# Optimization experiments

Hardware: AMD Instinct MI355X
Metric: run time of the kernel (lower is better)

## Reference

```python
import math
import jax, jax.numpy as jnp
import numpy as np

B, T, D, M, S = 2, 4096, 1024, 256, 8
BEAM = 4
TAU = 1.0


def setup_inputs() -> dict:
    key = jax.random.key(0)
    ks = jax.random.split(key, 24)
    std = 0.02
    inp = {
        "mu": jax.random.normal(ks[0], (B, T, D), jnp.float32),
        "lam": jax.random.uniform(ks[1], (B, T, D), jnp.float32),
        "pi": jax.random.uniform(ks[2], (B, T, 7), jnp.float32),
        "pi_write": jax.random.uniform(ks[3], (B, T, 1), jnp.float32),
        "Wq": jax.random.normal(ks[4], (M, D), jnp.float32) * std,
        "bq": jnp.zeros((M,), jnp.float32),
        "Wk": jax.random.normal(ks[5], (M, D), jnp.float32) * std,
        "bk": jnp.zeros((M,), jnp.float32),
        "Wv": jax.random.normal(ks[6], (M, D), jnp.float32) * std,
        "bv": jnp.zeros((M,), jnp.float32),
        "Wo": jax.random.normal(ks[7], (D, M), jnp.float32) * std,
        "bo": jnp.zeros((D,), jnp.float32),
        "Ws1": jax.random.normal(ks[8], (256, 2 * D + 7), jnp.float32) * std,
        "bs1": jnp.zeros((256,), jnp.float32),
        "Ws2": jax.random.normal(ks[9], (1, 256), jnp.float32) * std,
        "bs2": jnp.zeros((1,), jnp.float32),
        "Wsr": jax.random.normal(ks[10], (M, M), jnp.float32) * std,
        "bsr": jnp.zeros((M,), jnp.float32),
        "scratch_init": jax.random.normal(ks[11], (1, S, M), jnp.float32) * 0.02,
        "gate": jnp.float32(-5.0),
    }
    return inp


def _build_tree(k, v, w):
    """Causal binary tree of weighted span summaries. Level 0 = leaves."""
    levels = [(k, v, w)]
    while k.shape[1] > 1:
        n = k.shape[1]
        if n % 2 == 1:
            pad = ((0, 0), (0, 1), (0, 0))
            k = jnp.pad(k, pad); v = jnp.pad(v, pad); w = jnp.pad(w, pad)
        k1, k2 = k[:, 0::2], k[:, 1::2]
        v1, v2 = v[:, 0::2], v[:, 1::2]
        w1, w2 = w[:, 0::2], w[:, 1::2]
        tw = w1 + w2 + 1e-8
        k = (w1 * k1 + w2 * k2) / tw
        v = (w1 * v1 + w2 * v2) / tw
        w = tw
        levels.append((k, v, w))
    return levels


def _retrieve_at_level(q, keys, values, beam):
    Bq, Tq, Mq = q.shape
    n = keys.shape[1]
    scores = jnp.einsum('btm,bnm->btn', q, keys) / math.sqrt(Mq)
    if n <= Tq:  # causal: query i may only see slot j <= i
        mask = jnp.arange(n)[None, :] > jnp.arange(Tq)[:, None]
        scores = jnp.where(mask[None], -jnp.inf, scores)
    kk = min(beam, n)
    if n > kk:
        vals, idx = jax.lax.top_k(scores, kk)           # (B,T,k)
        p = jax.nn.softmax(vals, axis=-1)               # == softmax of scattered sparse scores
        v_sel = jnp.take_along_axis(values[:, None], idx[..., None], axis=2)  # (B,T,k,M)
        return jnp.einsum('btk,btkm->btm', p, v_sel)
    attn = jax.nn.softmax(scores, axis=-1)
    return jnp.einsum('btn,bnm->btm', attn, values)


def reference(mu, lam, pi, pi_write, Wq, bq, Wk, bk, Wv, bv, Wo, bo,
              Ws1, bs1, Ws2, bs2, Wsr, bsr, scratch_init, gate):
    # ---- write: build causal tree from detached keys/values ----
    mu_d = jax.lax.stop_gradient(mu)
    w0 = jax.lax.stop_gradient(pi_write)                # (B,T,1)
    k = mu_d @ Wk.T + bk
    v = mu_d @ Wv.T + bv
    tree = _build_tree(k, v, w0)

    # ---- read ----
    q = mu @ Wq.T + bq                                  # (B,T,M)
    log_var = -jnp.log(jnp.clip(lam, 1e-6))
    si = jnp.concatenate([mu, log_var, pi], axis=-1)    # (B,T,2D+7)
    h = si @ Ws1.T + bs1
    h = h * jax.nn.sigmoid(h)                           # SiLU
    s = jax.nn.sigmoid((h @ Ws2.T + bs2)[..., 0])       # (B,T)

    scratch = jnp.broadcast_to(scratch_init, (mu.shape[0], S, M))
    sq = q @ Wsr.T + bsr
    sattn = jax.nn.softmax(jnp.einsum('btm,bsm->bts', sq, scratch) / math.sqrt(M), axis=-1)
    scratch_ctx = jnp.einsum('bts,bsm->btm', sattn, scratch)

    level_ctx = [_retrieve_at_level(q, lk, lv, BEAM) for (lk, lv, _) in tree]
    level_stack = jnp.stack(level_ctx, axis=2)          # (B,T,L,M)
    L = level_stack.shape[2]
    level_idx = jnp.arange(L, dtype=mu.dtype)
    s_scaled = s[..., None] * (L - 1)                   # (B,T,1)
    kappa = jnp.exp(-0.5 * ((level_idx - s_scaled) / TAU) ** 2)
    kappa = kappa / jnp.clip(kappa.sum(axis=-1, keepdims=True), 1e-8)
    tree_ctx = jnp.einsum('btl,btlm->btm', kappa, level_stack)

    blend = s[..., None]
    combined = (1.0 - blend) * tree_ctx + blend * scratch_ctx
    out = combined @ Wo.T + bo
    return jax.nn.sigmoid(gate) * out                   # (B,T,D)
```

## Files before the change

### kernel.cpp

```cpp
#include <hip/hip_runtime.h>
#include <math.h>

#define TT 4096
#define BB 2
#define MMDIM 256
#define RTOT 8192
#define NSLICE 39

typedef __attribute__((ext_vector_type(8))) short short8_t;
typedef __attribute__((ext_vector_type(4))) float f32x4;

template<int WITH_GATE>
__global__ __launch_bounds__(256) void gemm_f32(
    const float* __restrict__ A, const float* __restrict__ W,
    const float* __restrict__ bias, const float* __restrict__ gate,
    float* __restrict__ C, int K, int N)
{
    __shared__ float As[16][68];
    __shared__ float Ws[16][68];
    const int tid = threadIdx.x;
    const int tx = tid & 15, ty = tid >> 4;
    const int r0 = blockIdx.x * 64, c0 = blockIdx.y * 64;
    const int lr = tid >> 2;
    const int lk = (tid & 3) << 2;

    float acc[4][4] = {};

    for (int k0 = 0; k0 < K; k0 += 16) {
        float4 av = *(const float4*)&A[(size_t)(r0 + lr) * K + k0 + lk];
        float4 wv = *(const float4*)&W[(size_t)(c0 + lr) * K + k0 + lk];
        As[lk + 0][lr] = av.x; As[lk + 1][lr] = av.y;
        As[lk + 2][lr] = av.z; As[lk + 3][lr] = av.w;
        Ws[lk + 0][lr] = wv.x; Ws[lk + 1][lr] = wv.y;
        Ws[lk + 2][lr] = wv.z; Ws[lk + 3][lr] = wv.w;
        __syncthreads();
        #pragma unroll
        for (int kk = 0; kk < 16; ++kk) {
            float4 a = *(const float4*)&As[kk][ty * 4];
            float4 b = *(const float4*)&Ws[kk][tx * 4];
            acc[0][0] += a.x * b.x; acc[0][1] += a.x * b.y; acc[0][2] += a.x * b.z; acc[0][3] += a.x * b.w;
            acc[1][0] += a.y * b.x; acc[1][1] += a.y * b.y; acc[1][2] += a.y * b.z; acc[1][3] += a.y * b.w;
            acc[2][0] += a.z * b.x; acc[2][1] += a.z * b.y; acc[2][2] += a.z * b.z; acc[2][3] += a.z * b.w;
            acc[3][0] += a.w * b.x; acc[3][1] += a.w * b.y; acc[3][2] += a.w * b.z; acc[3][3] += a.w * b.w;
        }
        __syncthreads();
    }

    float g = 1.f;
    if (WITH_GATE) g = 1.f / (1.f + expf(-gate[0]));
    #pragma unroll
    for (int i = 0; i < 4; ++i) {
        int row = r0 + ty * 4 + i;
        float4 o;
        o.x = (acc[i][0] + bias[c0 + tx * 4 + 0]) * g;
        o.y = (acc[i][1] + bias[c0 + tx * 4 + 1]) * g;
        o.z = (acc[i][2] + bias[c0 + tx * 4 + 2]) * g;
        o.w = (acc[i][3] + bias[c0 + tx * 4 + 3]) * g;
        *(float4*)&C[(size_t)row * N + c0 + tx * 4] = o;
    }
}

__device__ __forceinline__ unsigned short f2bf(float x)
{
    unsigned u = __float_as_uint(x);
    u += 0x7fffu + ((u >> 16) & 1u);
    return (unsigned short)(u >> 16);
}

__global__ __launch_bounds__(256) void convert_split(
    const float* __restrict__ src, unsigned short* __restrict__ hi,
    unsigned short* __restrict__ lo, int n4)
{
    int i = blockIdx.x * 256 + threadIdx.x;
    if (i >= n4) return;
    float4 x = ((const float4*)src)[i];
    ushort4 h, l;
    h.x = f2bf(x.x); l.x = f2bf(x.x - __uint_as_float((unsigned)h.x << 16));
    h.y = f2bf(x.y); l.y = f2bf(x.y - __uint_as_float((unsigned)h.y << 16));
    h.z = f2bf(x.z); l.z = f2bf(x.z - __uint_as_float((unsigned)h.z << 16));
    h.w = f2bf(x.w); l.w = f2bf(x.w - __uint_as_float((unsigned)h.w << 16));
    ((ushort4*)hi)[i] = h;
    ((ushort4*)lo)[i] = l;
}

__global__ __launch_bounds__(256) void pad_ws1_split(
    const float* __restrict__ src, unsigned short* __restrict__ hi,
    unsigned short* __restrict__ lo)
{
    const int r = blockIdx.x;
    for (int c = threadIdx.x; c < 2112; c += 256) {
        float v = (c < 2055) ? src[(size_t)r * 2055 + c] : 0.f;
        unsigned short h = f2bf(v);
        hi[(size_t)r * 2112 + c] = h;
        lo[(size_t)r * 2112 + c] = f2bf(v - __uint_as_float((unsigned)h << 16));
    }
}

template<int ASRC, int WITH_GATE>
__global__ __launch_bounds__(256) void gemm_mfma(
    const float* __restrict__ A, const float* __restrict__ lam,
    const float* __restrict__ pi,
    const unsigned short* __restrict__ Wh, const unsigned short* __restrict__ Wl,
    const float* __restrict__ bias, const float* __restrict__ gate,
    float* __restrict__ C, int K, int N)
{
    __shared__ unsigned short Ah[64][72], Al[64][72];
    __shared__ unsigned short Bh[128][72], Bl[128][72];
    const int tid = threadIdx.x;
    const int lane = tid & 63;
    const int wv = tid >> 6;
    const int r0 = blockIdx.x * 64;
    const int c0 = blockIdx.y * 128;

    f32x4 acc0[8] = {}, acc1[8] = {}, acc2[8] = {};

    const int arow = wv * 16 + (lane & 15);
    const int koff = (lane >> 4) * 8;

    for (int kc = 0; kc < K; kc += 64) {
        #pragma unroll
        for (int i = 0; i < 2; ++i) {
            int g = tid + i * 256;
            int row = g >> 3, gq = g & 7;
            float x[8];
            if (ASRC == 0) {
                float4 v0 = *(const float4*)&A[(size_t)(r0 + row) * K + kc + gq * 8];
                float4 v1 = *(const float4*)&A[(size_t)(r0 + row) * K + kc + gq * 8 + 4];
// ... 29 lines not shown
            *(short8_t*)&Bl[row][gq * 8] = *(const short8_t*)&Wl[(size_t)(c0 + row) * K + kc + gq * 8];
        }
        __syncthreads();
        #pragma unroll
        for (int kt = 0; kt < 2; ++kt) {
            short8_t afh = *(const short8_t*)&Ah[arow][kt * 32 + koff];
            short8_t afl = *(const short8_t*)&Al[arow][kt * 32 + koff];
            #pragma unroll
            for (int ct = 0; ct < 8; ++ct) {
                short8_t bh = *(const short8_t*)&Bh[ct * 16 + (lane & 15)][kt * 32 + koff];
                short8_t bl = *(const short8_t*)&Bl[ct * 16 + (lane & 15)][kt * 32 + koff];
                acc0[ct] = __builtin_amdgcn_mfma_f32_16x16x32_bf16(afh, bh, acc0[ct], 0, 0, 0);
                acc1[ct] = __builtin_amdgcn_mfma_f32_16x16x32_bf16(afl, bh, acc1[ct], 0, 0, 0);
                acc2[ct] = __builtin_amdgcn_mfma_f32_16x16x32_bf16(afh, bl, acc2[ct], 0, 0, 0);
            }
        }
        __syncthreads();
    }

    float g = 1.f;
    if (WITH_GATE) g = 1.f / (1.f + expf(-gate[0]));
    #pragma unroll
    for (int ct = 0; ct < 8; ++ct) {
        int col = c0 + ct * 16 + (lane & 15);
        float b = bias[col];
        #pragma unroll
        for (int r = 0; r < 4; ++r) {
            int row = r0 + wv * 16 + (lane >> 4) * 4 + r;
            C[(size_t)row * N + col] = (acc0[ct][r] + acc1[ct][r] + acc2[ct][r] + b) * g;
        }
    }
}

__global__ __launch_bounds__(256) void s_kernel(
    const float* __restrict__ h, const float* __restrict__ Ws2,
    const float* __restrict__ bs2, float* __restrict__ sb,
    float* __restrict__ kap)
{
    const int tid = threadIdx.x;
    const int wave = tid >> 6, lane = tid & 63;
    const int t = blockIdx.x * 4 + wave;

    float4 hv = *(const float4*)&h[(size_t)t * MMDIM + lane * 4];
    float4 wv = *(const float4*)&Ws2[lane * 4];
    float p = 0.f;
    p += (hv.x / (1.f + expf(-hv.x))) * wv.x;
    p += (hv.y / (1.f + expf(-hv.y))) * wv.y;
    p += (hv.z / (1.f + expf(-hv.z))) * wv.z;
    p += (hv.w / (1.f + expf(-hv.w))) * wv.w;
    #pragma unroll
    for (int o = 32; o; o >>= 1) p += __shfl_xor(p, o);

    float z = p + bs2[0];
    float s = 1.f / (1.f + expf(-z));
    float c = s * 12.f;
    float Z = 0.f;
    #pragma unroll
    for (int l = 0; l < 13; ++l) {
        float d = (float)l - c;
        Z += expf(-0.5f * d * d);
    }
    Z = fmaxf(Z, 1e-8f);
    if (lane < 13) {
        float d = (float)lane - c;
        kap[(size_t)t * 16 + lane] = (1.f - s) * expf(-0.5f * d * d) / Z;
    }
    if (lane == 0) sb[t] = s;
}

__global__ __launch_bounds__(256) void scratch_kernel(
    const float* __restrict__ sq, const float* __restrict__ scr,
    const float* __restrict__ sb, float* __restrict__ ctx)
{
    const int tid = threadIdx.x;
    const int wave = tid >> 6, lane = tid & 63;
    const int t = blockIdx.x * 4 + wave;

    float4 qv = *(const float4*)&sq[(size_t)t * MMDIM + lane * 4];
    float4 fr[8];
    float sc[8];
    #pragma unroll
    for (int s = 0; s < 8; ++s) {
        fr[s] = *(const float4*)&scr[s * MMDIM + lane * 4];
        sc[s] = qv.x * fr[s].x + qv.y * fr[s].y + qv.z * fr[s].z + qv.w * fr[s].w;
    }
    #pragma unroll
    for (int s = 0; s < 8; ++s) {
        #pragma unroll
        for (int o = 32; o; o >>= 1) sc[s] += __shfl_xor(sc[s], o);
        sc[s] *= 0.0625f;
    }
    float mx = sc[0];
    #pragma unroll
    for (int s = 1; s < 8; ++s) mx = fmaxf(mx, sc[s]);
    float sum = 0.f;
    #pragma unroll
    for (int s = 0; s < 8; ++s) { sc[s] = expf(sc[s] - mx); sum += sc[s]; }
    float inv = 1.f / sum;
    float blend = sb[t];
    float4 o = {0, 0, 0, 0};
    #pragma unroll
    for (int s = 0; s < 8; ++s) {
        float pp = sc[s] * inv;
        o.x += pp * fr[s].x; o.y += pp * fr[s].y;
        o.z += pp * fr[s].z; o.w += pp * fr[s].w;
    }
    o.x *= blend; o.y *= blend; o.z *= blend; o.w *= blend;
    *(float4*)&ctx[(size_t)t * MMDIM + lane * 4] = o;
}

__global__ __launch_bounds__(256) void wtree_kernel(
    const float* __restrict__ pw, float* __restrict__ wtree)
{
    __shared__ float wa[4096];
    __shared__ float wb2[2048];
    const int b = blockIdx.x;
    const int tid = threadIdx.x;
    for (int t = tid; t < 4096; t += 256) wa[t] = pw[b * 4096 + t];
    __syncthreads();
    int n = 4096, lvl = 1;
    float* cur = wa; float* nxt = wb2;
    while (n > 1) {
        int nout = n >> 1;
        int off = TT - (8192 >> lvl);
        for (int j = tid; j < nout; j += 256) {
            float t = cur[2 * j] + cur[2 * j + 1] + 1e-8f;
            nxt[j] = t;
            wtree[b * 4095 + off + j] = t;
        }
        __syncthreads();
        float* tmp = cur; cur = nxt; nxt = tmp;
        n = nout; ++lvl;
    }
}

__global__ __launch_bounds__(256) void tree_level(
    const float* __restrict__ kin, const float* __restrict__ vin,
    const float* __restrict__ win, float* __restrict__ kout,
    float* __restrict__ vout, int in_bs, int win_bs, int out_bs)
{
    const int j = blockIdx.x;
    const int b = blockIdx.y;
    const int tid = threadIdx.x;
    const float* wp = win + (size_t)b * win_bs;
    float w1 = wp[2 * j], w2 = wp[2 * j + 1];
    float tw = w1 + w2 + 1e-8f;
    size_t i1 = ((size_t)b * in_bs + 2 * j) * MMDIM + tid;
    size_t io = ((size_t)b * out_bs + j) * MMDIM + tid;
    kout[io] = (w1 * kin[i1] + w2 * kin[i1 + MMDIM]) / tw;
    vout[io] = (w1 * vin[i1] + w2 * vin[i1 + MMDIM]) / tw;
}

__global__ __launch_bounds__(256) void tree_deep(
    float* __restrict__ kt_, float* __restrict__ vt_,
    const float* __restrict__ wtree)
{
    __shared__ float kb[128][68];
    __shared__ float vb[128][68];
    const int tid = threadIdx.x;
    const int mc = blockIdx.x;
    const int b = blockIdx.y;
    const int wb = b * 4095;

    for (int idx = tid; idx < 64 * 64; idx += 256) {
        int j = idx >> 6, m = idx & 63;
        size_t gi = (size_t)(wb + 3968 + j) * MMDIM + mc * 64 + m;
        kb[j][m] = kt_[gi];
        vb[j][m] = vt_[gi];
    }
    __syncthreads();

    int pb = 0;
    for (int l = 7; l <= 12; ++l) {
        int nout = 4096 >> l;
        int cb = 128 - (128 >> (l - 6));
        int offm1 = TT - (8192 >> (l - 1));
        int offl  = TT - (8192 >> l);
        for (int idx = tid; idx < nout * 64; idx += 256) {
            int j = idx >> 6, m = idx & 63;
            float w1 = wtree[wb + offm1 + 2 * j];
            float w2 = wtree[wb + offm1 + 2 * j + 1];
            float tw = wtree[wb + offl + j];
            float kvv = (w1 * kb[pb + 2 * j][m] + w2 * kb[pb + 2 * j + 1][m]) / tw;
            float vvv = (w1 * vb[pb + 2 * j][m] + w2 * vb[pb + 2 * j + 1][m]) / tw;
            kb[cb + j][m] = kvv;
            vb[cb + j][m] = vvv;
            size_t go = (size_t)(wb + offl + j) * MMDIM + mc * 64 + m;
            kt_[go] = kvv;
            vt_[go] = vvv;
        }
        __syncthreads();
        pb = cb;
    }
}

__device__ __forceinline__ bool beats(float v, int id, float v2, int id2)
{
    return (v > v2) || (v == v2 && id < id2);
}

__device__ __forceinline__ void ins4(float v, int id, float tv[4], int ti[4])
{
    if (!beats(v, id, tv[3], ti[3])) return;
    tv[3] = v; ti[3] = id;
    #pragma unroll
    for (int s = 3; s > 0; --s) {
        if (beats(tv[s], ti[s], tv[s - 1], ti[s - 1])) {
            float fv = tv[s]; tv[s] = tv[s - 1]; tv[s - 1] = fv;
            int iv = ti[s]; ti[s] = ti[s - 1]; ti[s - 1] = iv;
        }
    }
}

__device__ __forceinline__ void ins5(float v, int id, float tv[5], int ti[5])
{
    if (!beats(v, id, tv[4], ti[4])) return;
    tv[4] = v; ti[4] = id;
    #pragma unroll
    for (int s = 4; s > 0; --s) {
        if (beats(tv[s], ti[s], tv[s - 1], ti[s - 1])) {
            float fv = tv[s]; tv[s] = tv[s - 1]; tv[s - 1] = fv;
            int iv = ti[s]; ti[s] = ti[s - 1]; ti[s - 1] = iv;
        }
    }
}

__device__ __forceinline__ void slice_map(int sid, int& level, int& c0)
{
    if (sid < 16)      { level = 0; c0 = sid << 8; }
    else if (sid < 24) { level = 1; c0 = (sid - 16) << 8; }
    else if (sid < 28) { level = 2; c0 = (sid - 24) << 8; }
    else if (sid < 30) { level = 3; c0 = (sid - 28) << 8; }
    else               { level = sid - 26; c0 = 0; }
}

__global__ __launch_bounds__(256) void topk_mfma(
    const unsigned short* __restrict__ qkh, const unsigned short* __restrict__ qkl,
    const unsigned short* __restrict__ kth, const unsigned short* __restrict__ ktl,
    float2* __restrict__ topw)
{
    __shared__ unsigned short kbh[32][264];
    __shared__ unsigned short kbl[32][264];

    const int tid = threadIdx.x;
    const int lane = tid & 63;
    const int wv = tid >> 6;
    const int r0 = blockIdx.x * 64;
    const int sid = blockIdx.y;
    const int b = r0 >> 12;
    const int t0 = r0 & 4095;

    int level, c0b;
    slice_map(sid, level, c0b);
    const int n = TT >> level;
    const int nv = min(min(n, t0 + 64), c0b + 256);

    if (c0b >= nv) {
        if (tid < 64) {
            float2 e = make_float2(-INFINITY, __int_as_float(0x7fffffff));
            #pragma unroll
            for (int s = 0; s < 5; ++s)
                topw[(size_t)(sid * 5 + s) * RTOT + r0 + tid] = e;
        }
        return;
    }

    const unsigned short* Kh;
    const unsigned short* Kl;
    if (level == 0) {
        Kh = qkh + (size_t)RTOT * MMDIM + (size_t)b * TT * MMDIM;
        Kl = qkl + (size_t)RTOT * MMDIM + (size_t)b * TT * MMDIM;
    } else {
        size_t off = (size_t)b * 4095 + (TT - (8192 >> level));
        Kh = kth + off * MMDIM;
        Kl = ktl + off * MMDIM;
    }

    const int arow = r0 + wv * 16 + (lane & 15);
    const int koff = (lane >> 4) * 8;
    short8_t ah[8], al[8];
    #pragma unroll
    for (int kt = 0; kt < 8; ++kt) {
        ah[kt] = *(const short8_t*)(qkh + (size_t)arow * MMDIM + kt * 32 + koff);
        al[kt] = *(const short8_t*)(qkl + (size_t)arow * MMDIM + kt * 32 + koff);
    }

    float tv[4][4];
    int ti[4][4];
    #pragma unroll
    for (int r = 0; r < 4; ++r)
        #pragma unroll
        for (int s = 0; s < 4; ++s) { tv[r][s] = -INFINITY; ti[r][s] = 0x7fffffff; }

    const int scol = tid >> 3;
    const int kseg = (tid & 7) * 32;

    for (int c0 = c0b; c0 < nv; c0 += 32) {
        {
            int cc = min(c0 + scol, n - 1);
            const unsigned short* gh = Kh + (size_t)cc * MMDIM + kseg;
            const unsigned short* gl = Kl + (size_t)cc * MMDIM + kseg;
            #pragma unroll
            for (int i = 0; i < 4; ++i) {
                *(short8_t*)&kbh[scol][kseg + i * 8] = *(const short8_t*)(gh + i * 8);
                *(short8_t*)&kbl[scol][kseg + i * 8] = *(const short8_t*)(gl + i * 8);
            }
        }
        __syncthreads();

        #pragma unroll
        for (int ct = 0; ct < 2; ++ct) {
            f32x4 a0 = {0.f, 0.f, 0.f, 0.f};
            f32x4 a1 = {0.f, 0.f, 0.f, 0.f};
            f32x4 a2 = {0.f, 0.f, 0.f, 0.f};
            const int bc = ct * 16 + (lane & 15);
            #pragma unroll
            for (int kt = 0; kt < 8; ++kt) {
                short8_t bh = *(const short8_t*)&kbh[bc][kt * 32 + koff];
                short8_t bl = *(const short8_t*)&kbl[bc][kt * 32 + koff];
                a0 = __builtin_amdgcn_mfma_f32_16x16x32_bf16(ah[kt], bh, a0, 0, 0, 0);
                a1 = __builtin_amdgcn_mfma_f32_16x16x32_bf16(al[kt], bh, a1, 0, 0, 0);
                a2 = __builtin_amdgcn_mfma_f32_16x16x32_bf16(ah[kt], bl, a2, 0, 0, 0);
            }
            const int col = c0 + bc;
            #pragma unroll
            for (int r = 0; r < 4; ++r) {
                int trow = t0 + wv * 16 + (lane >> 4) * 4 + r;
                float cand = (col <= trow && col < n)
                    ? (a0[r] + a1[r] + a2[r]) * 0.0625f : -INFINITY;
                if (__any(cand > tv[r][3])) ins4(cand, col, tv[r], ti[r]);
            }
        }
        __syncthreads();
    }

    #pragma unroll
    for (int r = 0; r < 4; ++r) {
        float v5[5]; int i5[5];
        #pragma unroll
        for (int s = 0; s < 4; ++s) { v5[s] = tv[r][s]; i5[s] = ti[r][s]; }
        v5[4] = -INFINITY; i5[4] = 0x7fffffff;
        #pragma unroll
        for (int pass = 0; pass < 4; ++pass) {
            int off = 1 << pass;
            float ov[5]; int oi[5];
            #pragma unroll
            for (int s = 0; s < 5; ++s) {
                ov[s] = __shfl_xor(v5[s], off);
                oi[s] = __shfl_xor(i5[s], off);
            }
            #pragma unroll
            for (int s = 0; s < 5; ++s) ins5(ov[s], oi[s], v5, i5);
        }
        if ((lane & 15) == 0) {
            int row = r0 + wv * 16 + (lane >> 4) * 4 + r;
            #pragma unroll
            for (int s = 0; s < 5; ++s)
                topw[(size_t)(sid * 5 + s) * RTOT + row] =
                    make_float2(v5[s], __int_as_float(i5[s]));
        }
    }
}

__global__ __launch_bounds__(256) void merge_gather(
    const float2* __restrict__ topw, const float* __restrict__ q,
    const float* __restrict__ kl0, const float* __restrict__ ktf,
    const float* __restrict__ vl0, const float* __restrict__ vtree,
    const float* __restrict__ kap, float* __restrict__ ctx)
{
    const int tid = threadIdx.x;
    const int lane = tid & 63;
    const int wv = __builtin_amdgcn_readfirstlane(tid >> 6);
    const int row = blockIdx.x * 4 + wv;
    const int b = row >> 12;

    float cr[4] = {0, 0, 0, 0};
    const float4 q4 = *(const float4*)&q[(size_t)row * MMDIM + lane * 4];

    for (int l = 0; l <= 12; ++l) {
        int s0, cnt;
        if (l == 0)      { s0 = 0;  cnt = 16; }
        else if (l == 1) { s0 = 16; cnt = 8; }
        else if (l == 2) { s0 = 24; cnt = 4; }
        else if (l == 3) { s0 = 28; cnt = 2; }
        else             { s0 = 26 + l; cnt = 1; }

        float tv[5]; int ti[5];
        #pragma unroll
        for (int s = 0; s < 5; ++s) { tv[s] = -INFINITY; ti[s] = 0x7fffffff; }
        for (int sl = 0; sl < cnt; ++sl) {
            #pragma unroll
            for (int s = 0; s < 5; ++s) {
// ... 81 lines not shown
    const float* bs2 = (const float*)d_in[15];
    const float* Wsr = (const float*)d_in[16];
    const float* bsr = (const float*)d_in[17];
    const float* scr = (const float*)d_in[18];
    const float* gate = (const float*)d_in[19];
    float* out = (float*)d_out;

    float* w = (float*)d_ws;
    const size_t RM = (size_t)RTOT * MMDIM;
    float* q_   = w;  w += RM;
    float* k_   = w;  w += RM;
    float* v_   = w;  w += RM;
    float* h_   = w;  w += RM;
    float* sq_  = w;  w += RM;
    float* ctx_ = w;  w += RM;
    float* sb_  = w;  w += RTOT;
    float* kap_ = w;  w += (size_t)RTOT * 16;
    float* kt_  = w;  w += (size_t)BB * 4095 * MMDIM;
    float* vt_  = w;  w += (size_t)BB * 4095 * MMDIM;
    float* wtree_ = w; w += (size_t)BB * 4095;
    unsigned short* qkh_ = (unsigned short*)w;  w += RM;
    unsigned short* qkl_ = (unsigned short*)w;  w += RM;
    unsigned short* kth_ = (unsigned short*)w;  w += (size_t)BB * 4095 * MMDIM / 2;
    unsigned short* ktl_ = (unsigned short*)w;  w += (size_t)BB * 4095 * MMDIM / 2;
    float2* topw = (float2*)w;  w += (size_t)NSLICE * 5 * RTOT * 2;
    unsigned short* w1h_ = (unsigned short*)w;  w += (size_t)256 * 2112 / 2;
    unsigned short* w1l_ = (unsigned short*)w;  w += (size_t)256 * 2112 / 2;
    unsigned short* wvh_ = (unsigned short*)w;  w += (size_t)256 * 1024 / 2;
    unsigned short* wvl_ = (unsigned short*)w;  w += (size_t)256 * 1024 / 2;
    unsigned short* wsrh_ = (unsigned short*)w; w += (size_t)256 * 256 / 2;
    unsigned short* wsrl_ = (unsigned short*)w; w += (size_t)256 * 256 / 2;
    unsigned short* woh_ = (unsigned short*)w;  w += (size_t)1024 * 256 / 2;
    unsigned short* wol_ = (unsigned short*)w;  w += (size_t)1024 * 256 / 2;

    pad_ws1_split<<<256, 256, 0, stream>>>(Ws1, w1h_, w1l_);
    convert_split<<<256, 256, 0, stream>>>(Wv, wvh_, wvl_, 65536);
    convert_split<<<64, 256, 0, stream>>>(Wsr, wsrh_, wsrl_, 16384);
    convert_split<<<256, 256, 0, stream>>>(Wo, woh_, wol_, 65536);

    gemm_f32<0><<<dim3(128, 4), 256, 0, stream>>>(mu, Wq, bq, nullptr, q_, 1024, 256);
    gemm_f32<0><<<dim3(128, 4), 256, 0, stream>>>(mu, Wk, bk, nullptr, k_, 1024, 256);
    gemm_mfma<0, 0><<<dim3(128, 2), 256, 0, stream>>>(mu, nullptr, nullptr, wvh_, wvl_,
                                                      bv, nullptr, v_, 1024, 256);
    gemm_mfma<1, 0><<<dim3(128, 2), 256, 0, stream>>>(mu, lam, pi, w1h_, w1l_,
                                                      bs1, nullptr, h_, 2112, 256);
    s_kernel<<<2048, 256, 0, stream>>>(h_, Ws2, bs2, sb_, kap_);
    gemm_mfma<0, 0><<<dim3(128, 2), 256, 0, stream>>>(q_, nullptr, nullptr, wsrh_, wsrl_,
                                                      bsr, nullptr, sq_, 256, 256);
    scratch_kernel<<<2048, 256, 0, stream>>>(sq_, scr, sb_, ctx_);

    wtree_kernel<<<BB, 256, 0, stream>>>(pw, wtree_);
    {
        const float* kin = k_; const float* vin = v_; const float* win = pw;
        int in_bs = TT, win_bs = TT;
        for (int l = 1; l <= 6; ++l) {
            int nout = TT >> l;
            int off = TT - (8192 >> l);
            float* ko = kt_ + (size_t)off * MMDIM;
            float* vo = vt_ + (size_t)off * MMDIM;
            tree_level<<<dim3(nout, BB), 256, 0, stream>>>(kin, vin, win, ko, vo,
                                                           in_bs, win_bs, 4095);
            kin = ko; vin = vo; win = wtree_ + off;
            in_bs = 4095; win_bs = 4095;
        }
    }
    tree_deep<<<dim3(4, BB), 256, 0, stream>>>(kt_, vt_, wtree_);

    convert_split<<<(int)((2 * RM / 4 + 255) / 256), 256, 0, stream>>>(
        q_, qkh_, qkl_, (int)(2 * RM / 4));
    convert_split<<<(int)(((size_t)BB * 4095 * MMDIM / 4 + 255) / 256), 256, 0, stream>>>(
        kt_, kth_, ktl_, (int)((size_t)BB * 4095 * MMDIM / 4));

    topk_mfma<<<dim3(128, NSLICE), 256, 0, stream>>>(qkh_, qkl_, kth_, ktl_, topw);
    merge_gather<<<2048, 256, 0, stream>>>(topw, q_, k_, kt_, v_, vt_, kap_, ctx_);
    gemm_mfma<0, 1><<<dim3(128, 8), 256, 0, stream>>>(ctx_, nullptr, nullptr, woh_, wol_,
                                                      bo, gate, out, 256, 1024);
}
```

Before: 873.2 us.

## Pack top-k keys into 64-bit ints, fuse tree levels, double topk block rows

The top-k insertion now stores each score and column together in one order-preserving 64-bit key, so comparisons are single integer compares and the shuffle merge moves one value per entry instead of two. The topk kernel processes 128 query rows per 512-thread block, so each staged K tile is reused across twice as many rows. The per-level tree_level launches for levels 2-6 are replaced by one tree_mid kernel that reduces a 64-leaf group in shared memory, removing five launches and the global round-trips between them. The unused gate template is dropped from gemm_f32. Risks are the larger block lowering occupancy, 64-bit shuffle cost, and the reproduction of tie-breaking through the packed key encoding.

```diff
diff --git a/kernel.cpp b/kernel.cpp
--- a/kernel.cpp
+++ b/kernel.cpp
@@ -10,11 +10,9 @@
 typedef __attribute__((ext_vector_type(8))) short short8_t;
 typedef __attribute__((ext_vector_type(4))) float f32x4;
 
-template<int WITH_GATE>
 __global__ __launch_bounds__(256) void gemm_f32(
     const float* __restrict__ A, const float* __restrict__ W,
-    const float* __restrict__ bias, const float* __restrict__ gate,
-    float* __restrict__ C, int K, int N)
+    const float* __restrict__ bias, float* __restrict__ C, int K, int N)
 {
     __shared__ float As[16][68];
     __shared__ float Ws[16][68];
@@ -46,16 +44,14 @@
         __syncthreads();
     }
 
-    float g = 1.f;
-    if (WITH_GATE) g = 1.f / (1.f + expf(-gate[0]));
     #pragma unroll
     for (int i = 0; i < 4; ++i) {
         int row = r0 + ty * 4 + i;
         float4 o;
-        o.x = (acc[i][0] + bias[c0 + tx * 4 + 0]) * g;
-        o.y = (acc[i][1] + bias[c0 + tx * 4 + 1]) * g;
-        o.z = (acc[i][2] + bias[c0 + tx * 4 + 2]) * g;
-        o.w = (acc[i][3] + bias[c0 + tx * 4 + 3]) * g;
+        o.x = acc[i][0] + bias[c0 + tx * 4 + 0];
+        o.y = acc[i][1] + bias[c0 + tx * 4 + 1];
+        o.z = acc[i][2] + bias[c0 + tx * 4 + 2];
+        o.w = acc[i][3] + bias[c0 + tx * 4 + 3];
         *(float4*)&C[(size_t)row * N + c0 + tx * 4] = o;
     }
 }
@@ -307,6 +303,51 @@
     vout[io] = (w1 * vin[i1] + w2 * vin[i1 + MMDIM]) / tw;
 }
 
+__global__ __launch_bounds__(256) void tree_mid(
+    float* __restrict__ kt_, float* __restrict__ vt_,
+    const float* __restrict__ wtree)
+{
+    __shared__ float kb[128][68];
+    __shared__ float vb[128][68];
+    const int tid = threadIdx.x;
+    const int g  = blockIdx.x >> 2;
+    const int mc = blockIdx.x & 3;
+    const int b  = blockIdx.y;
+    const int wb = b * 4095;
+
+    for (int idx = tid; idx < 64 * 64; idx += 256) {
+        int j = idx >> 6, m = idx & 63;
+        size_t gi = (size_t)(wb + g * 64 + j) * MMDIM + mc * 64 + m;
+        kb[j][m] = kt_[gi];
+        vb[j][m] = vt_[gi];
+    }
+    __syncthreads();
+
+    int pb = 0;
+    for (int l = 2; l <= 6; ++l) {
+        int nloc = 64 >> (l - 1);
+        int cb = 128 - (128 >> (l - 1));
+        int offm1 = TT - (8192 >> (l - 1));
+        int offl  = TT - (8192 >> l);
+        int gbase = g * nloc;
+        for (int idx = tid; idx < nloc * 64; idx += 256) {
+            int j = idx >> 6, m = idx & 63;
+            float w1 = wtree[wb + offm1 + (gbase + j) * 2];
+            float w2 = wtree[wb + offm1 + (gbase + j) * 2 + 1];
+            float tw = wtree[wb + offl + gbase + j];
+            float kvv = (w1 * kb[pb + 2 * j][m] + w2 * kb[pb + 2 * j + 1][m]) / tw;
+            float vvv = (w1 * vb[pb + 2 * j][m] + w2 * vb[pb + 2 * j + 1][m]) / tw;
+            kb[cb + j][m] = kvv;
+            vb[cb + j][m] = vvv;
+            size_t go = (size_t)(wb + offl + gbase + j) * MMDIM + mc * 64 + m;
+            kt_[go] = kvv;
+            vt_[go] = vvv;
+        }
+        __syncthreads();
+        pb = cb;
+    }
+}
+
 __global__ __launch_bounds__(256) void tree_deep(
     float* __restrict__ kt_, float* __restrict__ vt_,
     const float* __restrict__ wtree)
@@ -350,22 +391,50 @@
     }
 }
 
+__device__ __forceinline__ unsigned long long pack_key(float v, int col)
+{
+    unsigned u = __float_as_uint(v);
+    u ^= ((unsigned)((int)u >> 31)) | 0x80000000u;
+    return ((unsigned long long)u << 32) | (unsigned)(~col);
+}
+
+__device__ __forceinline__ void unpack_key(unsigned long long k, float& v, int& col)
+{
+    unsigned u = (unsigned)(k >> 32);
+    u ^= (u & 0x80000000u) ? 0x80000000u : 0xFFFFFFFFu;
+    v = __uint_as_float(u);
+    col = (int)(~(unsigned)k);
+}
+
+__device__ __forceinline__ unsigned long long shfl_xor_u64(unsigned long long v, int off)
+{
+    int lo = __shfl_xor((int)(unsigned)v, off);
+    int hi = __shfl_xor((int)(v >> 32), off);
+    return ((unsigned long long)(unsigned)hi << 32) | (unsigned)lo;
+}
+
+__device__ __forceinline__ void ins4u(unsigned long long k, unsigned long long t[4])
+{
+    if (k <= t[3]) return;
+    t[3] = k;
+    if (t[3] > t[2]) { unsigned long long x = t[2]; t[2] = t[3]; t[3] = x; }
+    if (t[2] > t[1]) { unsigned long long x = t[1]; t[1] = t[2]; t[2] = x; }
+    if (t[1] > t[0]) { unsigned long long x = t[0]; t[0] = t[1]; t[1] = x; }
+}
+
+__device__ __forceinline__ void ins5u(unsigned long long k, unsigned long long t[5])
+{
+    if (k <= t[4]) return;
+    t[4] = k;
+    if (t[4] > t[3]) { unsigned long long x = t[3]; t[3] = t[4]; t[4] = x; }
+    if (t[3] > t[2]) { unsigned long long x = t[2]; t[2] = t[3]; t[3] = x; }
+    if (t[2] > t[1]) { unsigned long long x = t[1]; t[1] = t[2]; t[2] = x; }
+    if (t[1] > t[0]) { unsigned long long x = t[0]; t[0] = t[1]; t[1] = x; }
+}
+
 __device__ __forceinline__ bool beats(float v, int id, float v2, int id2)
 {
     return (v > v2) || (v == v2 && id < id2);
-}
-
-__device__ __forceinline__ void ins4(float v, int id, float tv[4], int ti[4])
-{
-    if (!beats(v, id, tv[3], ti[3])) return;
-    tv[3] = v; ti[3] = id;
-    #pragma unroll
-    for (int s = 3; s > 0; --s) {
-        if (beats(tv[s], ti[s], tv[s - 1], ti[s - 1])) {
-            float fv = tv[s]; tv[s] = tv[s - 1]; tv[s - 1] = fv;
-            int iv = ti[s]; ti[s] = ti[s - 1]; ti[s - 1] = iv;
-        }
-    }
 }
 
 __device__ __forceinline__ void ins5(float v, int id, float tv[5], int ti[5])
@@ -390,7 +459,7 @@
     else               { level = sid - 26; c0 = 0; }
 }
 
-__global__ __launch_bounds__(256) void topk_mfma(
+__global__ __launch_bounds__(512) void topk_mfma(
     const unsigned short* __restrict__ qkh, const unsigned short* __restrict__ qkl,
     const unsigned short* __restrict__ kth, const unsigned short* __restrict__ ktl,
     float2* __restrict__ topw)
@@ -401,7 +470,7 @@
     const int tid = threadIdx.x;
     const int lane = tid & 63;
     const int wv = tid >> 6;
-    const int r0 = blockIdx.x * 64;
+    const int r0 = blockIdx.x * 128;
     const int sid = blockIdx.y;
     const int b = r0 >> 12;
     const int t0 = r0 & 4095;
@@ -409,10 +478,10 @@
     int level, c0b;
     slice_map(sid, level, c0b);
     const int n = TT >> level;
-    const int nv = min(min(n, t0 + 64), c0b + 256);
+    const int nv = min(min(n, t0 + 128), c0b + 256);
 
     if (c0b >= nv) {
-        if (tid < 64) {
+        if (tid < 128) {
             float2 e = make_float2(-INFINITY, __int_as_float(0x7fffffff));
             #pragma unroll
             for (int s = 0; s < 5; ++s)
@@ -441,26 +510,21 @@
         al[kt] = *(const short8_t*)(qkl + (size_t)arow * MMDIM + kt * 32 + koff);
     }
 
-    float tv[4][4];
-    int ti[4][4];
-    #pragma unroll
-    for (int r = 0; r < 4; ++r)
-        #pragma unroll
-        for (int s = 0; s < 4; ++s) { tv[r][s] = -INFINITY; ti[r][s] = 0x7fffffff; }
-
-    const int scol = tid >> 3;
-    const int kseg = (tid & 7) * 32;
+    unsigned long long tk[4][4] = {};
+    const int trow0 = t0 + wv * 16 + (lane >> 4) * 4;
+
+    const int scol = tid >> 4;
+    const int kseg = (tid & 15) * 16;
 
     for (int c0 = c0b; c0 < nv; c0 += 32) {
         {
             int cc = min(c0 + scol, n - 1);
             const unsigned short* gh = Kh + (size_t)cc * MMDIM + kseg;
             const unsigned short* gl = Kl + (size_t)cc * MMDIM + kseg;
-            #pragma unroll
-            for (int i = 0; i < 4; ++i) {
-                *(short8_t*)&kbh[scol][kseg + i * 8] = *(const short8_t*)(gh + i * 8);
-                *(short8_t*)&kbl[scol][kseg + i * 8] = *(const short8_t*)(gl + i * 8);
-            }
+            *(short8_t*)&kbh[scol][kseg]     = *(const short8_t*)gh;
+            *(short8_t*)&kbh[scol][kseg + 8] = *(const short8_t*)(gh + 8);
+            *(short8_t*)&kbl[scol][kseg]     = *(const short8_t*)gl;
+            *(short8_t*)&kbl[scol][kseg + 8] = *(const short8_t*)(gl + 8);
         }
         __syncthreads();
 
@@ -481,10 +545,10 @@
             const int col = c0 + bc;
             #pragma unroll
             for (int r = 0; r < 4; ++r) {
-                int trow = t0 + wv * 16 + (lane >> 4) * 4 + r;
-                float cand = (col <= trow && col < n)
-                    ? (a0[r] + a1[r] + a2[r]) * 0.0625f : -INFINITY;
-                if (__any(cand > tv[r][3])) ins4(cand, col, tv[r], ti[r]);
+                float sc = (a0[r] + a1[r] + a2[r]) * 0.0625f;
+                unsigned long long key =
+                    (col <= trow0 + r && col < n) ? pack_key(sc, col) : 0ull;
+                if (__any(key > tk[r][3])) ins4u(key, tk[r]);
             }
         }
         __syncthreads();
@@ -492,28 +556,33 @@
 
     #pragma unroll
     for (int r = 0; r < 4; ++r) {
-        float v5[5]; int i5[5];
-        #pragma unroll
-        for (int s = 0; s < 4; ++s) { v5[s] = tv[r][s]; i5[s] = ti[r][s]; }
-        v5[4] = -INFINITY; i5[4] = 0x7fffffff;
+        unsigned long long k5[5];
+        #pragma unroll
+        for (int s = 0; s < 4; ++s) k5[s] = tk[r][s];
+        k5[4] = 0ull;
         #pragma unroll
         for (int pass = 0; pass < 4; ++pass) {
             int off = 1 << pass;
-            float ov[5]; int oi[5];
-            #pragma unroll
-            for (int s = 0; s < 5; ++s) {
-                ov[s] = __shfl_xor(v5[s], off);
-                oi[s] = __shfl_xor(i5[s], off);
-            }
-            #pragma unroll
-            for (int s = 0; s < 5; ++s) ins5(ov[s], oi[s], v5, i5);
+            unsigned long long o[5];
+            #pragma unroll
+            for (int s = 0; s < 5; ++s) o[s] = shfl_xor_u64(k5[s], off);
+            #pragma unroll
+            for (int s = 0; s < 5; ++s) ins5u(o[s], k5);
         }
         if ((lane & 15) == 0) {
             int row = r0 + wv * 16 + (lane >> 4) * 4 + r;
             #pragma unroll
-            for (int s = 0; s < 5; ++s)
-                topw[(size_t)(sid * 5 + s) * RTOT + row] =
-                    make_float2(v5[s], __int_as_float(i5[s]));
+            for (int s = 0; s < 5; ++s) {
+                float2 e;
+                if (k5[s] == 0ull) {
+                    e = make_float2(-INFINITY, __int_as_float(0x7fffffff));
+                } else {
+                    float v; int c;
+                    unpack_key(k5[s], v, c);
+                    e = make_float2(v, __int_as_float(c));
+                }
+                topw[(size_t)(sid * 5 + s) * RTOT + row] = e;
+            }
         }
     }
 }
@@ -667,8 +736,8 @@
     convert_split<<<64, 256, 0, stream>>>(Wsr, wsrh_, wsrl_, 16384);
     convert_split<<<256, 256, 0, stream>>>(Wo, woh_, wol_, 65536);
 
-    gemm_f32<0><<<dim3(128, 4), 256, 0, stream>>>(mu, Wq, bq, nullptr, q_, 1024, 256);
-    gemm_f32<0><<<dim3(128, 4), 256, 0, stream>>>(mu, Wk, bk, nullptr, k_, 1024, 256);
+    gemm_f32<<<dim3(128, 4), 256, 0, stream>>>(mu, Wq, bq, q_, 1024, 256);
+    gemm_f32<<<dim3(128, 4), 256, 0, stream>>>(mu, Wk, bk, k_, 1024, 256);
     gemm_mfma<0, 0><<<dim3(128, 2), 256, 0, stream>>>(mu, nullptr, nullptr, wvh_, wvl_,
                                                       bv, nullptr, v_, 1024, 256);
     gemm_mfma<1, 0><<<dim3(128, 2), 256, 0, stream>>>(mu, lam, pi, w1h_, w1l_,
@@ -679,20 +748,9 @@
     scratch_kernel<<<2048, 256, 0, stream>>>(sq_, scr, sb_, ctx_);
 
     wtree_kernel<<<BB, 256, 0, stream>>>(pw, wtree_);
-    {
-        const float* kin = k_; const float* vin = v_; const float* win = pw;
-        int in_bs = TT, win_bs = TT;
-        for (int l = 1; l <= 6; ++l) {
-            int nout = TT >> l;
-            int off = TT - (8192 >> l);
-            float* ko = kt_ + (size_t)off * MMDIM;
-            float* vo = vt_ + (size_t)off * MMDIM;
-            tree_level<<<dim3(nout, BB), 256, 0, stream>>>(kin, vin, win, ko, vo,
-                                                           in_bs, win_bs, 4095);
-            kin = ko; vin = vo; win = wtree_ + off;
-            in_bs = 4095; win_bs = 4095;
-        }
-    }
+    tree_level<<<dim3(2048, BB), 256, 0, stream>>>(k_, v_, pw, kt_, vt_,
+                                                   TT, TT, 4095);
+    tree_mid<<<dim3(128, BB), 256, 0, stream>>>(kt_, vt_, wtree_);
     tree_deep<<<dim3(4, BB), 256, 0, stream>>>(kt_, vt_, wtree_);
 
     convert_split<<<(int)((2 * RM / 4 + 255) / 256), 256, 0, stream>>>(
@@ -700,7 +758,7 @@
     convert_split<<<(int)(((size_t)BB * 4095 * MMDIM / 4 + 255) / 256), 256, 0, stream>>>(
         kt_, kth_, ktl_, (int)((size_t)BB * 4095 * MMDIM / 4));
 
-    topk_mfma<<<dim3(128, NSLICE), 256, 0, stream>>>(qkh_, qkl_, kth_, ktl_, topw);
+    topk_mfma<<<dim3(64, NSLICE), 512, 0, stream>>>(qkh_, qkl_, kth_, ktl_, topw);
     merge_gather<<<2048, 256, 0, stream>>>(topw, q_, k_, kt_, v_, vt_, kap_, ctx_);
     gemm_mfma<0, 1><<<dim3(128, 8), 256, 0, stream>>>(ctx_, nullptr, nullptr, woh_, wol_,
                                                       bo, gate, out, 256, 1024);
```

After: 899.9 us. 1.03x slower.

## Fuse weight splits, Q/K GEMMs, s/scratch kernels, and tree levels into fewer launches

Applied to the files above, without the earlier changes.

Merges the four weight-splitting launches into one kernel and the separate Q and K FP32 GEMMs into one double-buffered GEMM that also emits the bf16 hi/lo split of q and k. The s and scratch kernels become a single kernel, which removes the sb round trip. The six per-level tree launches become one shared-memory tree_all kernel that writes the bf16 split inline, as tree_deep now does too, so the separate convert passes are gone. The aim is to cut launch overhead and redundant global traffic, at the cost of more complex kernels and a tree kernel that relies on large shared-memory buffers.

```diff
diff --git a/kernel.cpp b/kernel.cpp
--- a/kernel.cpp
+++ b/kernel.cpp
@@ -10,56 +10,6 @@
 typedef __attribute__((ext_vector_type(8))) short short8_t;
 typedef __attribute__((ext_vector_type(4))) float f32x4;
 
-template<int WITH_GATE>
-__global__ __launch_bounds__(256) void gemm_f32(
-    const float* __restrict__ A, const float* __restrict__ W,
-    const float* __restrict__ bias, const float* __restrict__ gate,
-    float* __restrict__ C, int K, int N)
-{
-    __shared__ float As[16][68];
-    __shared__ float Ws[16][68];
-    const int tid = threadIdx.x;
-    const int tx = tid & 15, ty = tid >> 4;
-    const int r0 = blockIdx.x * 64, c0 = blockIdx.y * 64;
-    const int lr = tid >> 2;
-    const int lk = (tid & 3) << 2;
-
-    float acc[4][4] = {};
-
-    for (int k0 = 0; k0 < K; k0 += 16) {
-        float4 av = *(const float4*)&A[(size_t)(r0 + lr) * K + k0 + lk];
-        float4 wv = *(const float4*)&W[(size_t)(c0 + lr) * K + k0 + lk];
-        As[lk + 0][lr] = av.x; As[lk + 1][lr] = av.y;
-        As[lk + 2][lr] = av.z; As[lk + 3][lr] = av.w;
-        Ws[lk + 0][lr] = wv.x; Ws[lk + 1][lr] = wv.y;
-        Ws[lk + 2][lr] = wv.z; Ws[lk + 3][lr] = wv.w;
-        __syncthreads();
-        #pragma unroll
-        for (int kk = 0; kk < 16; ++kk) {
-            float4 a = *(const float4*)&As[kk][ty * 4];
-            float4 b = *(const float4*)&Ws[kk][tx * 4];
-            acc[0][0] += a.x * b.x; acc[0][1] += a.x * b.y; acc[0][2] += a.x * b.z; acc[0][3] += a.x * b.w;
-            acc[1][0] += a.y * b.x; acc[1][1] += a.y * b.y; acc[1][2] += a.y * b.z; acc[1][3] += a.y * b.w;
-            acc[2][0] += a.z * b.x; acc[2][1] += a.z * b.y; acc[2][2] += a.z * b.z; acc[2][3] += a.z * b.w;
-            acc[3][0] += a.w * b.x; acc[3][1] += a.w * b.y; acc[3][2] += a.w * b.z; acc[3][3] += a.w * b.w;
-        }
-        __syncthreads();
-    }
-
-    float g = 1.f;
-    if (WITH_GATE) g = 1.f / (1.f + expf(-gate[0]));
-    #pragma unroll
-    for (int i = 0; i < 4; ++i) {
-        int row = r0 + ty * 4 + i;
-        float4 o;
-        o.x = (acc[i][0] + bias[c0 + tx * 4 + 0]) * g;
-        o.y = (acc[i][1] + bias[c0 + tx * 4 + 1]) * g;
-        o.z = (acc[i][2] + bias[c0 + tx * 4 + 2]) * g;
-        o.w = (acc[i][3] + bias[c0 + tx * 4 + 3]) * g;
-        *(float4*)&C[(size_t)row * N + c0 + tx * 4] = o;
-    }
-}
-
 __device__ __forceinline__ unsigned short f2bf(float x)
 {
     unsigned u = __float_as_uint(x);
@@ -67,12 +17,102 @@
     return (unsigned short)(u >> 16);
 }
 
-__global__ __launch_bounds__(256) void convert_split(
-    const float* __restrict__ src, unsigned short* __restrict__ hi,
-    unsigned short* __restrict__ lo, int n4)
-{
-    int i = blockIdx.x * 256 + threadIdx.x;
-    if (i >= n4) return;
+__global__ __launch_bounds__(256) void gemm_qk(
+    const float* __restrict__ mu, const float* __restrict__ Wq,
+    const float* __restrict__ bq, const float* __restrict__ Wk,
+    const float* __restrict__ bk, float* __restrict__ q_, float* __restrict__ k_,
+    unsigned short* __restrict__ qkh, unsigned short* __restrict__ qkl)
+{
+    __shared__ float As[2][8][68];
+    __shared__ float Ws[2][8][132];
+    const int tid = threadIdx.x;
+    const int tx = tid & 15;
+    const int ty = tid >> 4;
+    const int r0 = blockIdx.x * 64;
+    const int c0 = blockIdx.y * 128;
+    const bool isq = (c0 < 256);
+
+    const float* W = isq ? (Wq + (size_t)c0 * 1024)
+                         : (Wk + (size_t)(c0 - 256) * 1024);
+    const float* bias = isq ? (bq + c0) : (bk + (c0 - 256));
+
+    const bool isA = (tid < 128);
+    const int sArow = tid >> 1, sAk = (tid & 1) * 4;
+    const int sWrow = tid >> 1, sWk = (tid & 1) * 4;
+
+    float acc[4][8] = {};
+    float4 rA, rW;
+
+    if (isA) rA = *(const float4*)&mu[(size_t)(r0 + sArow) * 1024 + sAk];
+    rW = *(const float4*)&W[(size_t)sWrow * 1024 + sWk];
+    if (isA) {
+        As[0][sAk + 0][sArow] = rA.x; As[0][sAk + 1][sArow] = rA.y;
+        As[0][sAk + 2][sArow] = rA.z; As[0][sAk + 3][sArow] = rA.w;
+    }
+    Ws[0][sWk + 0][sWrow] = rW.x; Ws[0][sWk + 1][sWrow] = rW.y;
+    Ws[0][sWk + 2][sWrow] = rW.z; Ws[0][sWk + 3][sWrow] = rW.w;
+    __syncthreads();
+
+    int buf = 0;
+    for (int k0 = 0; k0 < 1024; k0 += 8) {
+        const bool has = (k0 + 8 < 1024);
+        if (has) {
+            if (isA) rA = *(const float4*)&mu[(size_t)(r0 + sArow) * 1024 + k0 + 8 + sAk];
+            rW = *(const float4*)&W[(size_t)sWrow * 1024 + k0 + 8 + sWk];
+        }
+        #pragma unroll
+        for (int kk = 0; kk < 8; ++kk) {
+            float4 a  = *(const float4*)&As[buf][kk][ty * 4];
+            float4 b0 = *(const float4*)&Ws[buf][kk][tx * 8];
+            float4 b1 = *(const float4*)&Ws[buf][kk][tx * 8 + 4];
+            float av[4] = {a.x, a.y, a.z, a.w};
+            float bv[8] = {b0.x, b0.y, b0.z, b0.w, b1.x, b1.y, b1.z, b1.w};
+            #pragma unroll
+            for (int i = 0; i < 4; ++i)
+                #pragma unroll
+                for (int j = 0; j < 8; ++j)
+                    acc[i][j] += av[i] * bv[j];
+        }
+        if (has) {
+            int nb = buf ^ 1;
+            if (isA) {
+                As[nb][sAk + 0][sArow] = rA.x; As[nb][sAk + 1][sArow] = rA.y;
+                As[nb][sAk + 2][sArow] = rA.z; As[nb][sAk + 3][sArow] = rA.w;
+            }
+            Ws[nb][sWk + 0][sWrow] = rW.x; Ws[nb][sWk + 1][sWrow] = rW.y;
+            Ws[nb][sWk + 2][sWrow] = rW.z; Ws[nb][sWk + 3][sWrow] = rW.w;
+        }
+        __syncthreads();
+        buf ^= 1;
+    }
+
+    const int lcol = (c0 & 255) + tx * 8;
+    #pragma unroll
+    for (int i = 0; i < 4; ++i) {
+        int row = r0 + ty * 4 + i;
+        float o[8];
+        #pragma unroll
+        for (int j = 0; j < 8; ++j) o[j] = acc[i][j] + bias[tx * 8 + j];
+        float* dst = isq ? &q_[(size_t)row * MMDIM + lcol]
+                         : &k_[(size_t)row * MMDIM + lcol];
+        *(float4*)dst       = make_float4(o[0], o[1], o[2], o[3]);
+        *(float4*)(dst + 4) = make_float4(o[4], o[5], o[6], o[7]);
+        size_t srow = isq ? (size_t)row : (size_t)(RTOT + row);
+        short8_t sh, sl;
+        #pragma unroll
+        for (int j = 0; j < 8; ++j) {
+            unsigned short h = f2bf(o[j]);
+            sh[j] = (short)h;
+            sl[j] = (short)f2bf(o[j] - __uint_as_float((unsigned)h << 16));
+        }
+        *(short8_t*)&qkh[srow * MMDIM + lcol] = sh;
+        *(short8_t*)&qkl[srow * MMDIM + lcol] = sl;
+    }
+}
+
+__device__ __forceinline__ void split4(const float* src, unsigned short* hi,
+                                       unsigned short* lo, int i)
+{
     float4 x = ((const float4*)src)[i];
     ushort4 h, l;
     h.x = f2bf(x.x); l.x = f2bf(x.x - __uint_as_float((unsigned)h.x << 16));
@@ -83,16 +123,30 @@
     ((ushort4*)lo)[i] = l;
 }
 
-__global__ __launch_bounds__(256) void pad_ws1_split(
-    const float* __restrict__ src, unsigned short* __restrict__ hi,
-    unsigned short* __restrict__ lo)
-{
-    const int r = blockIdx.x;
-    for (int c = threadIdx.x; c < 2112; c += 256) {
-        float v = (c < 2055) ? src[(size_t)r * 2055 + c] : 0.f;
-        unsigned short h = f2bf(v);
-        hi[(size_t)r * 2112 + c] = h;
-        lo[(size_t)r * 2112 + c] = f2bf(v - __uint_as_float((unsigned)h << 16));
+__global__ __launch_bounds__(256) void split_weights(
+    const float* __restrict__ Ws1, const float* __restrict__ Wv,
+    const float* __restrict__ Wsr, const float* __restrict__ Wo,
+    unsigned short* __restrict__ w1h, unsigned short* __restrict__ w1l,
+    unsigned short* __restrict__ wvh, unsigned short* __restrict__ wvl,
+    unsigned short* __restrict__ wsrh, unsigned short* __restrict__ wsrl,
+    unsigned short* __restrict__ woh, unsigned short* __restrict__ wol)
+{
+    const int bid = blockIdx.x;
+    const int tid = threadIdx.x;
+    if (bid < 256) {
+        int r = bid;
+        for (int c = tid; c < 2112; c += 256) {
+            float v = (c < 2055) ? Ws1[(size_t)r * 2055 + c] : 0.f;
+            unsigned short h = f2bf(v);
+            w1h[(size_t)r * 2112 + c] = h;
+            w1l[(size_t)r * 2112 + c] = f2bf(v - __uint_as_float((unsigned)h << 16));
+        }
+    } else if (bid < 512) {
+        split4(Wv, wvh, wvl, (bid - 256) * 256 + tid);
+    } else if (bid < 576) {
+        split4(Wsr, wsrh, wsrl, (bid - 512) * 256 + tid);
+    } else {
+        split4(Wo, woh, wol, (bid - 576) * 256 + tid);
     }
 }
 
@@ -188,10 +242,11 @@
     }
 }
 
-__global__ __launch_bounds__(256) void s_kernel(
+__global__ __launch_bounds__(256) void s_scratch_kernel(
     const float* __restrict__ h, const float* __restrict__ Ws2,
-    const float* __restrict__ bs2, float* __restrict__ sb,
-    float* __restrict__ kap)
+    const float* __restrict__ bs2, const float* __restrict__ sq,
+    const float* __restrict__ scr, float* __restrict__ kap,
+    float* __restrict__ ctx)
 {
     const int tid = threadIdx.x;
     const int wave = tid >> 6, lane = tid & 63;
@@ -221,47 +276,36 @@
         float d = (float)lane - c;
         kap[(size_t)t * 16 + lane] = (1.f - s) * expf(-0.5f * d * d) / Z;
     }
-    if (lane == 0) sb[t] = s;
-}
-
-__global__ __launch_bounds__(256) void scratch_kernel(
-    const float* __restrict__ sq, const float* __restrict__ scr,
-    const float* __restrict__ sb, float* __restrict__ ctx)
-{
-    const int tid = threadIdx.x;
-    const int wave = tid >> 6, lane = tid & 63;
-    const int t = blockIdx.x * 4 + wave;
 
     float4 qv = *(const float4*)&sq[(size_t)t * MMDIM + lane * 4];
     float4 fr[8];
     float sc[8];
     #pragma unroll
-    for (int s = 0; s < 8; ++s) {
-        fr[s] = *(const float4*)&scr[s * MMDIM + lane * 4];
-        sc[s] = qv.x * fr[s].x + qv.y * fr[s].y + qv.z * fr[s].z + qv.w * fr[s].w;
-    }
-    #pragma unroll
-    for (int s = 0; s < 8; ++s) {
-        #pragma unroll
-        for (int o = 32; o; o >>= 1) sc[s] += __shfl_xor(sc[s], o);
-        sc[s] *= 0.0625f;
+    for (int ss = 0; ss < 8; ++ss) {
+        fr[ss] = *(const float4*)&scr[ss * MMDIM + lane * 4];
+        sc[ss] = qv.x * fr[ss].x + qv.y * fr[ss].y + qv.z * fr[ss].z + qv.w * fr[ss].w;
+    }
+    #pragma unroll
+    for (int ss = 0; ss < 8; ++ss) {
+        #pragma unroll
+        for (int o = 32; o; o >>= 1) sc[ss] += __shfl_xor(sc[ss], o);
+        sc[ss] *= 0.0625f;
     }
     float mx = sc[0];
     #pragma unroll
-    for (int s = 1; s < 8; ++s) mx = fmaxf(mx, sc[s]);
+    for (int ss = 1; ss < 8; ++ss) mx = fmaxf(mx, sc[ss]);
     float sum = 0.f;
     #pragma unroll
-    for (int s = 0; s < 8; ++s) { sc[s] = expf(sc[s] - mx); sum += sc[s]; }
+    for (int ss = 0; ss < 8; ++ss) { sc[ss] = expf(sc[ss] - mx); sum += sc[ss]; }
     float inv = 1.f / sum;
-    float blend = sb[t];
     float4 o = {0, 0, 0, 0};
     #pragma unroll
-    for (int s = 0; s < 8; ++s) {
-        float pp = sc[s] * inv;
-        o.x += pp * fr[s].x; o.y += pp * fr[s].y;
-        o.z += pp * fr[s].z; o.w += pp * fr[s].w;
-    }
-    o.x *= blend; o.y *= blend; o.z *= blend; o.w *= blend;
+    for (int ss = 0; ss < 8; ++ss) {
+        float pp = sc[ss] * inv;
+        o.x += pp * fr[ss].x; o.y += pp * fr[ss].y;
+        o.z += pp * fr[ss].z; o.w += pp * fr[ss].w;
+    }
+    o.x *= s; o.y *= s; o.z *= s; o.w *= s;
     *(float4*)&ctx[(size_t)t * MMDIM + lane * 4] = o;
 }
 
@@ -290,26 +334,65 @@
     }
 }
 
-__global__ __launch_bounds__(256) void tree_level(
-    const float* __restrict__ kin, const float* __restrict__ vin,
-    const float* __restrict__ win, float* __restrict__ kout,
-    float* __restrict__ vout, int in_bs, int win_bs, int out_bs)
-{
-    const int j = blockIdx.x;
-    const int b = blockIdx.y;
-    const int tid = threadIdx.x;
-    const float* wp = win + (size_t)b * win_bs;
-    float w1 = wp[2 * j], w2 = wp[2 * j + 1];
-    float tw = w1 + w2 + 1e-8f;
-    size_t i1 = ((size_t)b * in_bs + 2 * j) * MMDIM + tid;
-    size_t io = ((size_t)b * out_bs + j) * MMDIM + tid;
-    kout[io] = (w1 * kin[i1] + w2 * kin[i1 + MMDIM]) / tw;
-    vout[io] = (w1 * vin[i1] + w2 * vin[i1 + MMDIM]) / tw;
+__global__ __launch_bounds__(256) void tree_all(
+    const float* __restrict__ kleaf, const float* __restrict__ vleaf,
+    const float* __restrict__ pw, const float* __restrict__ wtree,
+    float* __restrict__ kt_, float* __restrict__ vt_,
+    unsigned short* __restrict__ kth, unsigned short* __restrict__ ktl)
+{
+    __shared__ float kb[254][64];
+    __shared__ float vb[254][64];
+    const int tid = threadIdx.x;
+    const int g  = blockIdx.x >> 2;
+    const int mc = blockIdx.x & 3;
+    const int b  = blockIdx.y;
+    const int wb = b * 4095;
+
+    for (int idx = tid; idx < 128 * 64; idx += 256) {
+        int j = idx >> 6, m = idx & 63;
+        size_t gi = ((size_t)b * TT + g * 128 + j) * MMDIM + mc * 64 + m;
+        kb[j][m] = kleaf[gi];
+        vb[j][m] = vleaf[gi];
+    }
+    __syncthreads();
+
+    int pb = 0, cb = 128;
+    for (int l = 1; l <= 6; ++l) {
+        int nloc = 64 >> (l - 1);
+        int offl = TT - (8192 >> l);
+        int gbase = g * nloc;
+        for (int idx = tid; idx < nloc * 64; idx += 256) {
+            int j = idx >> 6, m = idx & 63;
+            float w1, w2;
+            if (l == 1) {
+                w1 = pw[b * 4096 + (gbase + j) * 2];
+                w2 = pw[b * 4096 + (gbase + j) * 2 + 1];
+            } else {
+                int offm1 = TT - (8192 >> (l - 1));
+                w1 = wtree[wb + offm1 + (gbase + j) * 2];
+                w2 = wtree[wb + offm1 + (gbase + j) * 2 + 1];
+            }
+            float tw = wtree[wb + offl + gbase + j];
+            float kvv = (w1 * kb[pb + 2 * j][m] + w2 * kb[pb + 2 * j + 1][m]) / tw;
+            float vvv = (w1 * vb[pb + 2 * j][m] + w2 * vb[pb + 2 * j + 1][m]) / tw;
+            kb[cb + j][m] = kvv;
+            vb[cb + j][m] = vvv;
+            size_t go = (size_t)(wb + offl + gbase + j) * MMDIM + mc * 64 + m;
+            kt_[go] = kvv;
+            vt_[go] = vvv;
+            unsigned short hh = f2bf(kvv);
+            kth[go] = hh;
+            ktl[go] = f2bf(kvv - __uint_as_float((unsigned)hh << 16));
+        }
+        __syncthreads();
+        pb = cb; cb += nloc;
+    }
 }
 
 __global__ __launch_bounds__(256) void tree_deep(
     float* __restrict__ kt_, float* __restrict__ vt_,
-    const float* __restrict__ wtree)
+    const float* __restrict__ wtree,
+    unsigned short* __restrict__ kth, unsigned short* __restrict__ ktl)
 {
     __shared__ float kb[128][68];
     __shared__ float vb[128][68];
@@ -344,6 +427,9 @@
             size_t go = (size_t)(wb + offl + j) * MMDIM + mc * 64 + m;
             kt_[go] = kvv;
             vt_[go] = vvv;
+            unsigned short hh = f2bf(kvv);
+            kth[go] = hh;
+            ktl[go] = f2bf(kvv - __uint_as_float((unsigned)hh << 16));
         }
         __syncthreads();
         pb = cb;
@@ -661,44 +747,26 @@
     unsigned short* wsrl_ = (unsigned short*)w; w += (size_t)256 * 256 / 2;
     unsigned short* woh_ = (unsigned short*)w;  w += (size_t)1024 * 256 / 2;
     unsigned short* wol_ = (unsigned short*)w;  w += (size_t)1024 * 256 / 2;
-
-    pad_ws1_split<<<256, 256, 0, stream>>>(Ws1, w1h_, w1l_);
-    convert_split<<<256, 256, 0, stream>>>(Wv, wvh_, wvl_, 65536);
-    convert_split<<<64, 256, 0, stream>>>(Wsr, wsrh_, wsrl_, 16384);
-    convert_split<<<256, 256, 0, stream>>>(Wo, woh_, wol_, 65536);
-
-    gemm_f32<0><<<dim3(128, 4), 256, 0, stream>>>(mu, Wq, bq, nullptr, q_, 1024, 256);
-    gemm_f32<0><<<dim3(128, 4), 256, 0, stream>>>(mu, Wk, bk, nullptr, k_, 1024, 256);
+    (void)sb_;
+
+    split_weights<<<832, 256, 0, stream>>>(Ws1, Wv, Wsr, Wo,
+                                           w1h_, w1l_, wvh_, wvl_,
+                                           wsrh_, wsrl_, woh_, wol_);
+
+    gemm_qk<<<dim3(128, 4), 256, 0, stream>>>(mu, Wq, bq, Wk, bk,
+                                              q_, k_, qkh_, qkl_);
     gemm_mfma<0, 0><<<dim3(128, 2), 256, 0, stream>>>(mu, nullptr, nullptr, wvh_, wvl_,
                                                       bv, nullptr, v_, 1024, 256);
     gemm_mfma<1, 0><<<dim3(128, 2), 256, 0, stream>>>(mu, lam, pi, w1h_, w1l_,
                                                       bs1, nullptr, h_, 2112, 256);
-    s_kernel<<<2048, 256, 0, stream>>>(h_, Ws2, bs2, sb_, kap_);
     gemm_mfma<0, 0><<<dim3(128, 2), 256, 0, stream>>>(q_, nullptr, nullptr, wsrh_, wsrl_,
                                                       bsr, nullptr, sq_, 256, 256);
-    scratch_kernel<<<2048, 256, 0, stream>>>(sq_, scr, sb_, ctx_);
+    s_scratch_kernel<<<2048, 256, 0, stream>>>(h_, Ws2, bs2, sq_, scr, kap_, ctx_);
 
     wtree_kernel<<<BB, 256, 0, stream>>>(pw, wtree_);
-    {
-        const float* kin = k_; const float* vin = v_; const float* win = pw;
-        int in_bs = TT, win_bs = TT;
-        for (int l = 1; l <= 6; ++l) {
-            int nout = TT >> l;
-            int off = TT - (8192 >> l);
-            float* ko = kt_ + (size_t)off * MMDIM;
-            float* vo = vt_ + (size_t)off * MMDIM;
-            tree_level<<<dim3(nout, BB), 256, 0, stream>>>(kin, vin, win, ko, vo,
-                                                           in_bs, win_bs, 4095);
-            kin = ko; vin = vo; win = wtree_ + off;
-            in_bs = 4095; win_bs = 4095;
-        }
-    }
-    tree_deep<<<dim3(4, BB), 256, 0, stream>>>(kt_, vt_, wtree_);
-
-    convert_split<<<(int)((2 * RM / 4 + 255) / 256), 256, 0, stream>>>(
-        q_, qkh_, qkl_, (int)(2 * RM / 4));
-    convert_split<<<(int)(((size_t)BB * 4095 * MMDIM / 4 + 255) / 256), 256, 0, stream>>>(
-        kt_, kth_, ktl_, (int)((size_t)BB * 4095 * MMDIM / 4));
+    tree_all<<<dim3(128, BB), 256, 0, stream>>>(k_, v_, pw, wtree_, kt_, vt_,
+                                                kth_, ktl_);
+    tree_deep<<<dim3(4, BB), 256, 0, stream>>>(kt_, vt_, wtree_, kth_, ktl_);
 
     topk_mfma<<<dim3(128, NSLICE), 256, 0, stream>>>(qkh_, qkl_, kth_, ktl_, topw);
     merge_gather<<<2048, 256, 0, stream>>>(topw, q_, k_, kt_, v_, vt_, kap_, ctx_);
```

New measurement: 825.7 us. 5.4% less time.
